# Optimization experiments

Measured on AMD Instinct MI355X. Metric: run time of the kernel, lower is better.

## Reference

```python
import jax, jax.numpy as jnp
import numpy as np

DIM = 4096        # HypervectorEngine.DIMENSION
N_SAMPLES = 100   # linspace sample count in signal_to_hv
SPARSITY = 0.5    # get_sparse_hv default


def setup_inputs() -> dict:
    key = jax.random.key(0)
    # signal values in [0,1) -> val_seeds = round(signal*1000) in [0,1000]
    signal = jax.random.uniform(key, (512, 8192), dtype=jnp.float32)
    return {"signal": signal}


def _from_seed(base_key, seed):
    # Deterministic counter-based +/-1 bit-vector generation (JAX analogue of
    # torch.Generator.manual_seed(seed) + randint(0,2)). seed is masked to 32 bits
    # implicitly by int32 arithmetic.
    k = jax.random.fold_in(base_key, seed)
    bits = jax.random.bernoulli(k, 0.5, (DIM,)).astype(jnp.float32)
    return bits * 2.0 - 1.0


def reference(signal):
    B, L = signal.shape
    base_key = jax.random.key(42)

    # --- signal_to_hv (vectorized over batch and the 100 samples) ---
    idx = jnp.linspace(0.0, L - 1, N_SAMPLES).astype(jnp.int32)        # [100]
    sampled = signal[:, idx]                                           # [B,100]
    val_seeds = jnp.round(sampled * 1000.0).astype(jnp.int32)          # [B,100]
    pos = jnp.arange(N_SAMPLES, dtype=jnp.int32)                       # [100]
    seeds = jnp.bitwise_xor(pos[None, :], val_seeds)                   # [B,100]

    gen = jax.vmap(jax.vmap(lambda s: _from_seed(base_key, s)))
    hvs = gen(seeds)                                                   # [B,100,DIM]
    combined = jnp.sum(hvs, axis=1)                                    # [B,DIM] raw float HV

    # --- get_sparse_hv: keep top-|hv| half, set to sign, zero elsewhere ---
    n_key = int(DIM * SPARSITY)
    _, top_idx = jax.lax.top_k(jnp.abs(combined), n_key)               # [B,n_key]
    signs = jnp.sign(jnp.take_along_axis(combined, top_idx, axis=1))   # [B,n_key]
    sparse = jnp.zeros_like(combined)
    batch_idx = jnp.arange(B)[:, None]
    sparse = sparse.at[batch_idx, top_idx].set(signs)
    return sparse
```

## Files before the change

kernel.cpp:

```cpp
#include <hip/hip_runtime.h>
#include <stdint.h>


#define B_ROWS 512
#define SIG_L  8192
#define DIM    4096
#define NS     100
#define NKEY   2048
#define NSEED  1024

__device__ __forceinline__ void tf2x32(uint32_t k0, uint32_t k1,
                                       uint32_t& x0, uint32_t& x1) {
  const uint32_t k2 = k0 ^ k1 ^ 0x1BD11BDAu;
  x0 += k0; x1 += k1;
#define TF_RND(r) { x0 += x1; x1 = (x1 << (r)) | (x1 >> (32 - (r))); x1 ^= x0; }
  TF_RND(13) TF_RND(15) TF_RND(26) TF_RND(6)
  x0 += k1; x1 += k2 + 1u;
  TF_RND(17) TF_RND(29) TF_RND(16) TF_RND(24)
  x0 += k2; x1 += k0 + 2u;
  TF_RND(13) TF_RND(15) TF_RND(26) TF_RND(6)
  x0 += k0; x1 += k1 + 3u;
  TF_RND(17) TF_RND(29) TF_RND(16) TF_RND(24)
  x0 += k1; x1 += k2 + 4u;
  TF_RND(13) TF_RND(15) TF_RND(26) TF_RND(6)
  x0 += k2; x1 += k0 + 5u;
#undef TF_RND
}

__device__ __forceinline__ uint32_t rbits32(uint32_t k0, uint32_t k1, uint32_t i) {
  uint32_t x0 = 0u, x1 = i;
  tf2x32(k0, k1, x0, x1);
  return x0 ^ x1;
}

__global__ __launch_bounds__(256) void build_table_kernel(uint16_t* __restrict__ tbl16) {
  const int seed = blockIdx.x;
  __shared__ uint32_t kk[2];
  if (threadIdx.x == 0) {
    uint32_t x0 = 0u, x1 = (uint32_t)seed;
    tf2x32(0u, 42u, x0, x1);
    kk[0] = x0; kk[1] = x1;
  }
  __syncthreads();
  const uint32_t k0 = kk[0], k1 = kk[1];
  const int base = threadIdx.x * 16;
  uint32_t bits16 = 0;
#pragma unroll
  for (int k = 0; k < 16; ++k) {
    uint32_t b = rbits32(k0, k1, (uint32_t)(base + k)) >> 31;
    bits16 |= b << k;
  }
  tbl16[seed * 256 + threadIdx.x] = (uint16_t)bits16;
}

__global__ __launch_bounds__(512) void row_kernel_t(const float* __restrict__ signal,
                                                    const uint32_t* __restrict__ tbl32,
                                                    float* __restrict__ out) {
  const int b = blockIdx.x;
  const int t = threadIdx.x;
  const int j = t & 127;
  const int g = t >> 7;
  __shared__ int      sseed[NS];
  __shared__ int      hist[101];
  __shared__ int      wsum[8];
  __shared__ int      TQ[2];
  __shared__ uint32_t red[512 * 9];

  if (t < 101) hist[t] = 0;
  if (t < NS) {
    const float step = 8191.0f / 99.0f;
    float idxf = (float)t * step;
    int   idx  = (int)idxf;
    float v    = signal[b * SIG_L + idx];
    int   val  = __float2int_rn(v * 1000.0f);
    sseed[t] = t ^ val;
  }
  __syncthreads();

  uint32_t c[8];
#pragma unroll
  for (int q = 0; q < 8; ++q) c[q] = 0;
#pragma unroll 5
  for (int s = g; s < NS; s += 4) {
    const uint32_t m = tbl32[(sseed[s] << 7) + j];
#pragma unroll
    for (int q = 0; q < 8; ++q)
      c[q] += (((m >> (4 * q)) & 0xFu) * 0x00204081u) & 0x01010101u;
  }
#pragma unroll
  for (int q = 0; q < 8; ++q) red[t * 9 + q] = c[q];
  __syncthreads();

  if (t < 128) {
#pragma unroll
    for (int q = 0; q < 8; ++q) {
      uint32_t s0 = red[(j       ) * 9 + q] + red[(j + 128) * 9 + q];
      uint32_t s1 = red[(j + 256) * 9 + q] + red[(j + 384) * 9 + q];
      red[j * 9 + q] = s0 + s1;
    }
  }
  __syncthreads();

  const uint32_t cw0 = red[(t >> 2) * 9 + 2 * (t & 3)];
  const uint32_t cw1 = red[(t >> 2) * 9 + 2 * (t & 3) + 1];
  int acc[8];
#pragma unroll
  for (int k = 0; k < 4; ++k) {
    acc[k]     = NS - 2 * (int)((cw0 >> (8 * k)) & 0xFFu);
    acc[k + 4] = NS - 2 * (int)((cw1 >> (8 * k)) & 0xFFu);
  }

#pragma unroll
  for (int k = 0; k < 8; ++k) {
    int a = acc[k] < 0 ? -acc[k] : acc[k];
    atomicAdd(&hist[a], 1);
  }
  __syncthreads();

  if (t < 101) {
    int cum = 0;
    for (int x = t + 1; x <= 100; ++x) cum += hist[x];
    if (cum < NKEY && cum + hist[t] >= NKEY) { TQ[0] = t; TQ[1] = NKEY - cum; }
  }
  __syncthreads();
  const int T = TQ[0];
  const int Q = TQ[1];

  int cnt = 0;
#pragma unroll
  for (int k = 0; k < 8; ++k) {
    int a = acc[k] < 0 ? -acc[k] : acc[k];
    cnt += (a == T);
  }
  const int lane = t & 63, wv = t >> 6;
  int sc = cnt;
#pragma unroll
  for (int off = 1; off < 64; off <<= 1) {
    int n = __shfl_up(sc, off, 64);
    if (lane >= off) sc += n;
  }
  if (lane == 63) wsum[wv] = sc;
  __syncthreads();
  int prefix = sc - cnt;
  for (int w = 0; w < wv; ++w) prefix += wsum[w];

  float o[8];
#pragma unroll
  for (int k = 0; k < 8; ++k) {
    int   v = acc[k];
    int   a = v < 0 ? -v : v;
    float sg = v > 0 ? 1.0f : (v < 0 ? -1.0f : 0.0f);
    float r = 0.0f;
    if (a > T) {
      r = sg;
    } else if (a == T) {
      if (prefix < Q) r = sg;
      prefix++;
    }
    o[k] = r;
  }
  float4* op = (float4*)(out + (size_t)b * DIM + t * 8);
  op[0] = make_float4(o[0], o[1], o[2], o[3]);
  op[1] = make_float4(o[4], o[5], o[6], o[7]);
}

__global__ __launch_bounds__(512) void row_kernel_f(const float* __restrict__ signal,
                                                    float* __restrict__ out) {
  const int b = blockIdx.x;
  const int t = threadIdx.x;
  __shared__ uint32_t sk0[NS], sk1[NS];
  __shared__ int      hist[101];
  __shared__ int      wsum[8];
  __shared__ int      TQ[2];

  if (t < 101) hist[t] = 0;
  if (t < NS) {
    const float step = 8191.0f / 99.0f;
    int   idx  = (int)((float)t * step);
    float v    = signal[b * SIG_L + idx];
    int   val  = __float2int_rn(v * 1000.0f);
    int   sd   = t ^ val;
    uint32_t x0 = 0u, x1 = (uint32_t)sd;
    tf2x32(0u, 42u, x0, x1);
    sk0[t] = x0; sk1[t] = x1;
  }
  __syncthreads();

  uint32_t c_lo = 0, c_hi = 0;
  for (int s = 0; s < NS; ++s) {
    uint32_t m = 0;
    const uint32_t k0 = sk0[s], k1 = sk1[s];
    for (int jj = 0; jj < 8; ++jj)
      m |= (rbits32(k0, k1, (uint32_t)(8 * t + jj)) >> 31) << jj;
    c_lo += ((m & 0xFu) * 0x00204081u) & 0x01010101u;
    c_hi += ((m >> 4)   * 0x00204081u) & 0x01010101u;
  }
  int acc[8];
#pragma unroll
  for (int k = 0; k < 4; ++k) {
    acc[k]     = NS - 2 * (int)((c_lo >> (8 * k)) & 0xFFu);
    acc[k + 4] = NS - 2 * (int)((c_hi >> (8 * k)) & 0xFFu);
  }
#pragma unroll
  for (int k = 0; k < 8; ++k) {
    int a = acc[k] < 0 ? -acc[k] : acc[k];
    atomicAdd(&hist[a], 1);
  }
  __syncthreads();
  if (t < 101) {
    int cum = 0;
    for (int x = t + 1; x <= 100; ++x) cum += hist[x];
    if (cum < NKEY && cum + hist[t] >= NKEY) { TQ[0] = t; TQ[1] = NKEY - cum; }
  }
  __syncthreads();
  const int T = TQ[0];
  const int Q = TQ[1];
  int cnt = 0;
#pragma unroll
  for (int k = 0; k < 8; ++k) {
    int a = acc[k] < 0 ? -acc[k] : acc[k];
    cnt += (a == T);
  }
  const int lane = t & 63, wv = t >> 6;
  int sc = cnt;
#pragma unroll
  for (int off = 1; off < 64; off <<= 1) {
    int n = __shfl_up(sc, off, 64);
    if (lane >= off) sc += n;
  }
  if (lane == 63) wsum[wv] = sc;
  __syncthreads();
  int prefix = sc - cnt;
  for (int w = 0; w < wv; ++w) prefix += wsum[w];
  float o[8];
#pragma unroll
  for (int k = 0; k < 8; ++k) {
    int   v = acc[k];
    int   a = v < 0 ? -v : v;
    float sg = v > 0 ? 1.0f : (v < 0 ? -1.0f : 0.0f);
    float r = 0.0f;
    if (a > T) r = sg;
    else if (a == T) { if (prefix < Q) r = sg; prefix++; }
    o[k] = r;
  }
  float4* op = (float4*)(out + (size_t)b * DIM + t * 8);
  op[0] = make_float4(o[0], o[1], o[2], o[3]);
  op[1] = make_float4(o[4], o[5], o[6], o[7]);
}

extern "C" void kernel_launch(void* const* d_in, const int* in_sizes, int n_in,
                              void* d_out, int out_size, void* d_ws, size_t ws_size,
                              hipStream_t stream) {
  (void)in_sizes; (void)n_in; (void)out_size;
  const float* signal = (const float*)d_in[0];
  float* out = (float*)d_out;
  const size_t table_bytes = (size_t)NSEED * (DIM / 8);

  if (ws_size >= table_bytes) {
    build_table_kernel<<<NSEED, 256, 0, stream>>>((uint16_t*)d_ws);
    row_kernel_t<<<B_ROWS, 512, 0, stream>>>(signal, (const uint32_t*)d_ws, out);
  } else {
    row_kernel_f<<<B_ROWS, 512, 0, stream>>>(signal, out);
  }
}
```

Before: 82.41 us.

## Use bit-sliced counters and a privatized histogram with wave-scan threshold search

The per-seed popcount accumulation now uses a 5-bit bit-sliced ripple counter (XOR/AND) in place of unpacking eight nibble groups on every sample. The per-lane counts are expanded into byte counters only once, after the loop. The histogram is split into four copies, one per thread group, and indexed by a/2, relying on |acc| always being even since NS is even. The threshold search now runs as a single-wave suffix scan over 51 bins instead of a quadratic serial loop. This trades a little expansion work at the end for much less ALU work in the hot loop and less atomic contention.

Measured after the change: 78.04 us. -5.3%, faster.

```diff
diff --git a/kernel.cpp b/kernel.cpp
--- a/kernel.cpp
+++ b/kernel.cpp
@@ -61,12 +61,12 @@
   const int j = t & 127;
   const int g = t >> 7;
   __shared__ int      sseed[NS];
-  __shared__ int      hist[101];
+  __shared__ int      hist4[4 * 51];
   __shared__ int      wsum[8];
   __shared__ int      TQ[2];
   __shared__ uint32_t red[512 * 9];
 
-  if (t < 101) hist[t] = 0;
+  if (t < 4 * 51) hist4[t] = 0;
   if (t < NS) {
     const float step = 8191.0f / 99.0f;
     float idxf = (float)t * step;
@@ -77,18 +77,26 @@
   }
   __syncthreads();
 
-  uint32_t c[8];
-#pragma unroll
-  for (int q = 0; q < 8; ++q) c[q] = 0;
+  uint32_t p0 = 0, p1 = 0, p2 = 0, p3 = 0, p4 = 0;
 #pragma unroll 5
   for (int s = g; s < NS; s += 4) {
     const uint32_t m = tbl32[(sseed[s] << 7) + j];
-#pragma unroll
-    for (int q = 0; q < 8; ++q)
-      c[q] += (((m >> (4 * q)) & 0xFu) * 0x00204081u) & 0x01010101u;
-  }
-#pragma unroll
-  for (int q = 0; q < 8; ++q) red[t * 9 + q] = c[q];
+    uint32_t c0 = p0 & m;  p0 ^= m;
+    uint32_t c1 = p1 & c0; p1 ^= c0;
+    uint32_t c2 = p2 & c1; p2 ^= c1;
+    uint32_t c3 = p3 & c2; p3 ^= c2;
+    p4 ^= c3;
+  }
+
+#pragma unroll
+  for (int q = 0; q < 8; ++q) {
+    uint32_t e  =  (((p0 >> (4 * q)) & 0xFu) * 0x00204081u) & 0x01010101u;
+    e += ((((p1 >> (4 * q)) & 0xFu) * 0x00204081u) & 0x01010101u) << 1;
+    e += ((((p2 >> (4 * q)) & 0xFu) * 0x00204081u) & 0x01010101u) << 2;
+    e += ((((p3 >> (4 * q)) & 0xFu) * 0x00204081u) & 0x01010101u) << 3;
+    e += ((((p4 >> (4 * q)) & 0xFu) * 0x00204081u) & 0x01010101u) << 4;
+    red[t * 9 + q] = e;
+  }
   __syncthreads();
 
   if (t < 128) {
@@ -113,14 +121,21 @@
 #pragma unroll
   for (int k = 0; k < 8; ++k) {
     int a = acc[k] < 0 ? -acc[k] : acc[k];
-    atomicAdd(&hist[a], 1);
-  }
-  __syncthreads();
-
-  if (t < 101) {
-    int cum = 0;
-    for (int x = t + 1; x <= 100; ++x) cum += hist[x];
-    if (cum < NKEY && cum + hist[t] >= NKEY) { TQ[0] = t; TQ[1] = NKEY - cum; }
+    atomicAdd(&hist4[g * 51 + (a >> 1)], 1);
+  }
+  __syncthreads();
+
+  if (t < 64) {
+    int cnt = 0;
+    if (t < 51) cnt = hist4[t] + hist4[51 + t] + hist4[102 + t] + hist4[153 + t];
+    int S = cnt;
+#pragma unroll
+    for (int off = 1; off < 64; off <<= 1) {
+      int n = __shfl_down(S, off, 64);
+      if (t + off < 64) S += n;
+    }
+    int Sx = S - cnt;
+    if (Sx < NKEY && S >= NKEY) { TQ[0] = 2 * t; TQ[1] = NKEY - Sx; }
   }
   __syncthreads();
   const int T = TQ[0];
```
